# Kernel optimization log

Hardware: AMD Instinct MI355X
Metric: run time of the kernel (lower is better)

Reference implementation:

```python
import jax, jax.numpy as jnp
import numpy as np

N = 80000   # active voxels
G = 64      # voxel grid side
K = 27      # 3x3x3 kernel taps


def _build_coord_maps():
    """Random unique voxel coords in a G^3 grid; 27-tap neighbor index map (-1 = missing)."""
    rng = np.random.default_rng(0)
    flat = rng.choice(G ** 3, size=N, replace=False).astype(np.int64)
    coords = np.stack(np.unravel_index(flat, (G, G, G)), axis=1)  # (N,3)
    order = np.argsort(flat)
    skeys = flat[order]
    offs = [(dx, dy, dz) for dx in (-1, 0, 1) for dy in (-1, 0, 1) for dz in (-1, 0, 1)]
    nbr = np.full((K, N), -1, np.int32)
    for k, (dx, dy, dz) in enumerate(offs):
        nc = coords + np.array([dx, dy, dz])
        inb = np.all((nc >= 0) & (nc < G), axis=1)
        nkey = nc[:, 0] * G * G + nc[:, 1] * G + nc[:, 2]
        pos = np.clip(np.searchsorted(skeys, nkey), 0, N - 1)
        hit = inb & (skeys[pos] == nkey)
        nbr[k] = np.where(hit, order[pos], -1)
    return nbr


_W_SPECS = [('a1w', (27, 96, 64)), ('a2w', (64, 64)), ('a3w', (27, 64, 64)), ('a4w', (64, 64)),
            ('b1w', (27, 256, 64)), ('b2w', (64, 64)), ('b3w', (27, 64, 32)), ('b4w', (32, 32)),
            ('c1w', (27, 96, 128)), ('c2w', (128, 128)), ('c3w', (128, 128))]
_BN_SPECS = [('a1', 64), ('a2', 64), ('a3', 64), ('a4', 64),
             ('b1', 64), ('b2', 64), ('b3', 32), ('b4', 32),
             ('c1', 128), ('c2', 128), ('c3', 128)]


def setup_inputs() -> dict:
    key = jax.random.key(0)
    ks = jax.random.split(key, 64)
    inp = {
        'feat3d': jax.random.normal(ks[0], (N, 96), jnp.float32),
        'feat2d': jax.random.normal(ks[1], (N, 256), jnp.float32),
    }
    i = 2
    for name, shp in _W_SPECS:
        fan = float(np.prod(shp[:-1]))
        inp[name] = jax.random.normal(ks[i], shp, jnp.float32) * (1.0 / np.sqrt(fan))
        i += 1
    for pre, c in _BN_SPECS:  # folded eval-mode BN: y = x*scale + shift
        inp[pre + 's'] = 1.0 + 0.1 * jax.random.normal(ks[i], (c,), jnp.float32)
        inp[pre + 'b'] = 0.1 * jax.random.normal(ks[i + 1], (c,), jnp.float32)
        i += 2
    inp['nbr_idx'] = jnp.asarray(_build_coord_maps())
    inp['align_idx'] = jnp.arange(N, dtype=jnp.int32)  # 2D/3D share coordinates -> exact match
    return inp


def _sconv(x, W, nbr):
    """Sparse 3x3x3 conv: per-tap masked gather + GEMM, accumulated (gather-GEMM-scatter)."""
    out = jnp.zeros((x.shape[0], W.shape[-1]), x.dtype)
    for k in range(W.shape[0]):
        idx = nbr[k]
        g = jnp.where((idx >= 0)[:, None], x[jnp.maximum(idx, 0)], 0.0)
        out = out + g @ W[k]
    return out


def _bnrelu(x, s, b):
    return jax.nn.relu(x * s + b)


def reference(feat3d, feat2d,
              a1w, a2w, a3w, a4w, b1w, b2w, b3w, b4w, c1w, c2w, c3w,
              a1s, a1b, a2s, a2b, a3s, a3b, a4s, a4b,
              b1s, b1b, b2s, b2b, b3s, b3b, b4s, b4b,
              c1s, c1b, c2s, c2b, c3s, c3b,
              nbr_idx, align_idx):
    # 3D branch: 96 -> 64 (dropout = identity in eval)
    x = _bnrelu(_sconv(feat3d, a1w, nbr_idx), a1s, a1b)
    x = _bnrelu(x @ a2w, a2s, a2b)
    x = _bnrelu(_sconv(x, a3w, nbr_idx), a3s, a3b)
    x3 = _bnrelu(x @ a4w, a4s, a4b)
    # 2D branch: 256 -> 32
    y = _bnrelu(_sconv(feat2d, b1w, nbr_idx), b1s, b1b)
    y = _bnrelu(y @ b2w, b2s, b2b)
    y = _bnrelu(_sconv(y, b3w, nbr_idx), b3s, b3b)
    y2 = _bnrelu(y @ b4w, b4s, b4b)
    # features_at_coordinates: exact-match gather at the 3D coords, NaN/Inf -> 0
    ya = y2[align_idx]
    ya = jnp.where(jnp.isfinite(ya), ya, 0.0)
    # fusion: concat 64+32=96 -> 128
    z = jnp.concatenate([x3, ya], axis=1)
    z = _bnrelu(_sconv(z, c1w, nbr_idx), c1s, c1b)
    z = _bnrelu(z @ c2w, c2s, c2b)
    z = _bnrelu(z @ c3w, c3s, c3b)
    return z
```

## Files before the change

kernel.cpp:

```cpp
#include <hip/hip_runtime.h>

typedef __bf16 bf16;
typedef __bf16 bf16x8 __attribute__((ext_vector_type(8)));
typedef __bf16 bf16x4 __attribute__((ext_vector_type(4)));
typedef float  f32x4  __attribute__((ext_vector_type(4)));

__global__ void f2b_kernel(const float* __restrict__ src, bf16* __restrict__ dst, int n4) {
    int i = blockIdx.x * 256 + threadIdx.x;
    if (i >= n4) return;
    float4 v = ((const float4*)src)[i];
    bf16x4 o = { (bf16)v.x, (bf16)v.y, (bf16)v.z, (bf16)v.w };
    ((bf16x4*)dst)[i] = o;
}

__global__ void swz_kernel(const float* __restrict__ W, bf16* __restrict__ Wf,
                           int cin, int cout, int total) {
    int e = blockIdx.x * 256 + threadIdx.x;
    if (e >= total) return;
    int per_tap = cin * cout;
    int tap = e / per_tap;
    int t2  = e - tap * per_tap;
    int ntc = cout >> 4;
    int s   = t2 / (ntc * 512);
    int r3  = t2 - s * (ntc * 512);
    int nt  = r3 >> 9;
    int L   = (r3 & 511) >> 3;
    int j   = r3 & 7;
    int k   = s * 32 + (L >> 4) * 8 + j;
    int col = nt * 16 + (L & 15);
    Wf[e] = (bf16)W[((size_t)tap * cin + k) * cout + col];
}

template<int CIN, int C1, int TAPS, int KTILE, int C2, int C3>
__global__ __launch_bounds__(256, 3) void layer_kernel(
    const bf16* __restrict__ X,
    const bf16* __restrict__ W1,
    const bf16* __restrict__ W2,
    const bf16* __restrict__ W3,
    const int*  __restrict__ nbr,
    const float* __restrict__ sc1, const float* __restrict__ sh1,
    const float* __restrict__ sc2, const float* __restrict__ sh2,
    const float* __restrict__ sc3, const float* __restrict__ sh3,
    bf16* __restrict__ Y, float* __restrict__ Yf,
    int ystride, int yoff, int n, int nblocks)
{
    constexpr int M    = 128;
    constexpr int NT1  = C1 / 16;
    constexpr int WR1  = 4;
    constexpr int WC1  = (NT1 >= 2) ? NT1 / 2 : 1;
    constexpr int KH   = CIN / KTILE;
    constexpr int KS   = KTILE / 32;
    constexpr int CH   = KTILE / 8;
    constexpr int SREG = KTILE / 16;
    constexpr int AST  = KTILE + 8;
    constexpr int ABUF = M * AST;
    constexpr int ABY  = 2 * ABUF * 2;
    constexpr int LS1  = C1 + 8;
    constexpr int LS2  = C2 + 8;
    constexpr int L1BY = M * LS1 * 2;
    constexpr int L2BY = (C3 > 0) ? M * LS2 * 2 : 0;
    constexpr int SBY  = (ABY > L1BY ? (ABY > L2BY ? ABY : L2BY)
                                     : (L1BY > L2BY ? L1BY : L2BY));

    __shared__ __align__(16) char smem[SBY];
    __shared__ int idxs[TAPS * M];
    bf16* As = (bf16*)smem;

    const int tid = threadIdx.x;

    const int bq  = nblocks >> 3, br = nblocks & 7;
    const int bx  = blockIdx.x & 7, bs = blockIdx.x >> 3;
    const int sb  = bx * bq + (bx < br ? bx : br) + bs;
    const int base = sb * M;

    const int lane  = tid & 63;
    const int wv    = tid >> 6;
    const int m16   = lane & 15;
    const int quad  = lane >> 4;
    const int wrow1 = wv & 1;
    const int wcol1 = wv >> 1;

    for (int e = tid; e < TAPS * M; e += 256)
        idxs[e] = nbr[(e >> 7) * n + base + (e & (M - 1))];
    __syncthreads();

    int rr[SREG], cof[SREG], lofs[SREG];
#pragma unroll
    for (int j = 0; j < SREG; ++j) {
        int e = tid + 256 * j;
        rr[j]   = e / CH;
        int c   = e - rr[j] * CH;
        cof[j]  = c * 8;
        lofs[j] = rr[j] * AST + c * 8;
    }

    float4 sreg[SREG];
    auto issue_loads = [&](int kh, int t) {
#pragma unroll
        for (int j = 0; j < SREG; ++j) {
            int idx = idxs[t * M + rr[j]];
            float4 val = {0.f, 0.f, 0.f, 0.f};
            if (idx >= 0) val = *(const float4*)(X + (size_t)idx * CIN + kh * KTILE + cof[j]);
            sreg[j] = val;
        }
    };
    auto store_lds = [&](int buf) {
#pragma unroll
        for (int j = 0; j < SREG; ++j)
            *(float4*)(&As[buf * ABUF + lofs[j]]) = sreg[j];
    };

    f32x4 acc1[WR1][WC1];
#pragma unroll
    for (int r = 0; r < WR1; ++r)
#pragma unroll
        for (int c = 0; c < WC1; ++c) acc1[r][c] = (f32x4){0.f, 0.f, 0.f, 0.f};

    issue_loads(0, 0);
    store_lds(0);

    int it = 0;
    for (int kh = 0; kh < KH; ++kh)
        for (int t = 0; t < TAPS; ++t, ++it) {
            __syncthreads();

            const bf16* wt = W1 + (size_t)t * (CIN * C1);
            bf16x8 bfr[KS][WC1];
#pragma unroll
            for (int s = 0; s < KS; ++s)
#pragma unroll
                for (int c = 0; c < WC1; ++c)
                    bfr[s][c] = *(const bf16x8*)(wt + ((kh * KS + s) * NT1 + wcol1 * WC1 + c) * 512 + lane * 8);

            int t2 = t + 1, kh2 = kh;
            if (t2 == TAPS) { t2 = 0; kh2 = kh + 1; }
            const bool more = (kh2 < KH);
            if (more) issue_loads(kh2, t2);

            const int buf = it & 1;
#pragma unroll
            for (int s = 0; s < KS; ++s) {
                bf16x8 a[WR1];
#pragma unroll
                for (int r = 0; r < WR1; ++r)
                    a[r] = *(const bf16x8*)(&As[buf * ABUF + ((wrow1 * WR1 + r) * 16 + m16) * AST + s * 32 + quad * 8]);
#pragma unroll
                for (int r = 0; r < WR1; ++r)
#pragma unroll
                    for (int c = 0; c < WC1; ++c)
                        acc1[r][c] = __builtin_amdgcn_mfma_f32_16x16x32_bf16(a[r], bfr[s][c], acc1[r][c], 0, 0, 0);
            }

            if (more) store_lds(buf ^ 1);
        }

    __syncthreads();
    bf16* Lt1 = (bf16*)smem;
#pragma unroll
    for (int c = 0; c < WC1; ++c) {
        int col = (wcol1 * WC1 + c) * 16 + m16;
        float s1 = sc1[col], h1 = sh1[col];
#pragma unroll
        for (int r = 0; r < WR1; ++r) {
            int row0 = (wrow1 * WR1 + r) * 16 + quad * 4;
#pragma unroll
            for (int i = 0; i < 4; ++i) {
                float v = acc1[r][c][i] * s1 + h1;
                v = v > 0.f ? v : 0.f;
                Lt1[(row0 + i) * LS1 + col] = (bf16)v;
            }
        }
    }
    __syncthreads();

    constexpr int NT2 = C2 / 16;
    constexpr int WR2 = 4;
    constexpr int WC2 = (NT2 >= 2) ? NT2 / 2 : 1;
    constexpr int KS2 = C1 / 32;
    const int wrow2 = wv & 1, wcol2 = wv >> 1;

    f32x4 acc2[WR2][WC2];
#pragma unroll
    for (int r = 0; r < WR2; ++r)
#pragma unroll
        for (int c = 0; c < WC2; ++c) acc2[r][c] = (f32x4){0.f, 0.f, 0.f, 0.f};

#pragma unroll
    for (int s = 0; s < KS2; ++s) {
        bf16x8 a[WR2], bw[WC2];
#pragma unroll
        for (int r = 0; r < WR2; ++r)
            a[r] = *(const bf16x8*)(&Lt1[((wrow2 * WR2 + r) * 16 + m16) * LS1 + s * 32 + quad * 8]);
#pragma unroll
        for (int c = 0; c < WC2; ++c)
            bw[c] = *(const bf16x8*)(W2 + ((s * NT2 + wcol2 * WC2 + c) * 512 + lane * 8));
#pragma unroll
        for (int r = 0; r < WR2; ++r)
#pragma unroll
            for (int c = 0; c < WC2; ++c)
                acc2[r][c] = __builtin_amdgcn_mfma_f32_16x16x32_bf16(a[r], bw[c], acc2[r][c], 0, 0, 0);
    }

    if constexpr (C3 == 0) {
#pragma unroll
        for (int c = 0; c < WC2; ++c) {
            int col = (wcol2 * WC2 + c) * 16 + m16;
            float s2 = sc2[col], h2 = sh2[col];
#pragma unroll
            for (int r = 0; r < WR2; ++r) {
                int row0 = base + (wrow2 * WR2 + r) * 16 + quad * 4;
#pragma unroll
                for (int i = 0; i < 4; ++i) {
                    float v = acc2[r][c][i] * s2 + h2;
                    v = v > 0.f ? v : 0.f;
                    size_t off = (size_t)(row0 + i) * ystride + yoff + col;
                    if (Yf) Yf[off] = v;
                    else    Y[off] = (bf16)v;
                }
            }
        }
    } else {
        __syncthreads();
        bf16* Lt2 = (bf16*)smem;
#pragma unroll
        for (int c = 0; c < WC2; ++c) {
            int col = (wcol2 * WC2 + c) * 16 + m16;
            float s2 = sc2[col], h2 = sh2[col];
#pragma unroll
            for (int r = 0; r < WR2; ++r) {
                int row0 = (wrow2 * WR2 + r) * 16 + quad * 4;
#pragma unroll
                for (int i = 0; i < 4; ++i) {
                    float v = acc2[r][c][i] * s2 + h2;
                    v = v > 0.f ? v : 0.f;
                    Lt2[(row0 + i) * LS2 + col] = (bf16)v;
                }
            }
        }
        __syncthreads();

        constexpr int C3v = (C3 > 0) ? C3 : 16;
        constexpr int NT3 = C3v / 16;
        constexpr int WR3 = 4;
        constexpr int WC3 = (NT3 >= 2) ? NT3 / 2 : 1;
        constexpr int KS3 = C2 / 32;
        const int wrow3 = wv & 1, wcol3 = wv >> 1;

        f32x4 acc3[WR3][WC3];
#pragma unroll
        for (int r = 0; r < WR3; ++r)
#pragma unroll
            for (int c = 0; c < WC3; ++c) acc3[r][c] = (f32x4){0.f, 0.f, 0.f, 0.f};

#pragma unroll
        for (int s = 0; s < KS3; ++s) {
            bf16x8 a[WR3], bw[WC3];
#pragma unroll
            for (int r = 0; r < WR3; ++r)
                a[r] = *(const bf16x8*)(&Lt2[((wrow3 * WR3 + r) * 16 + m16) * LS2 + s * 32 + quad * 8]);
#pragma unroll
            for (int c = 0; c < WC3; ++c)
                bw[c] = *(const bf16x8*)(W3 + ((s * NT3 + wcol3 * WC3 + c) * 512 + lane * 8));
#pragma unroll
            for (int r = 0; r < WR3; ++r)
#pragma unroll
                for (int c = 0; c < WC3; ++c)
                    acc3[r][c] = __builtin_amdgcn_mfma_f32_16x16x32_bf16(a[r], bw[c], acc3[r][c], 0, 0, 0);
        }

#pragma unroll
        for (int c = 0; c < WC3; ++c) {
            int col = (wcol3 * WC3 + c) * 16 + m16;
            float s3 = sc3[col], h3 = sh3[col];
#pragma unroll
            for (int r = 0; r < WR3; ++r) {
                int row0 = base + (wrow3 * WR3 + r) * 16 + quad * 4;
#pragma unroll
                for (int i = 0; i < 4; ++i) {
                    float v = acc3[r][c][i] * s3 + h3;
                    v = v > 0.f ? v : 0.f;
                    size_t off = (size_t)(row0 + i) * ystride + yoff + col;
                    if (Yf) Yf[off] = v;
                    else    Y[off] = (bf16)v;
                }
            }
        }
    }
}

__global__ void concat_kernel(const bf16* __restrict__ y2, const int* __restrict__ align,
                              bf16* __restrict__ z, int n) {
    int e = blockIdx.x * 256 + threadIdx.x;
    if (e >= n * 32) return;
    int i = e >> 5, c = e & 31;
    int a = align[i];
    float v = (float)y2[(size_t)a * 32 + c];
    unsigned u = __builtin_bit_cast(unsigned, v);
    if ((u & 0x7f800000u) == 0x7f800000u) v = 0.f;
    z[(size_t)i * 96 + 64 + c] = (bf16)v;
}

extern "C" void kernel_launch(void* const* d_in, const int* in_sizes, int n_in,
                              void* d_out, int out_size, void* d_ws, size_t ws_size,
                              hipStream_t stream) {
    const float* feat3d = (const float*)d_in[0];
    const float* feat2d = (const float*)d_in[1];
    const float* Wsrc[11];
    for (int i = 0; i < 11; ++i) Wsrc[i] = (const float*)d_in[2 + i];
    const float* bn[22];
    for (int i = 0; i < 22; ++i) bn[i] = (const float*)d_in[13 + i];
    const int* nbr   = (const int*)d_in[35];
    const int* align = (const int*)d_in[36];
    float* out = (float*)d_out;

    const int n = in_sizes[0] / 96;

    char* ws = (char*)d_ws;
    size_t off = 0;
    auto alloc = [&](size_t bytes) -> void* {
        void* p = ws + off;
        off = (off + bytes + 255) & ~(size_t)255;
        return p;
    };
    bf16* F3 = (bf16*)alloc((size_t)n * 96 * 2);
    bf16* F2 = (bf16*)alloc((size_t)n * 256 * 2);
    static const int wt_taps[11] = {27, 1, 27, 1, 27, 1, 27, 1, 27, 1, 1};
    static const int wt_cin[11]  = {96, 64, 64, 64, 256, 64, 64, 32, 96, 128, 128};
    static const int wt_cout[11] = {64, 64, 64, 64, 64, 64, 32, 32, 128, 128, 128};
    bf16* Wf[11];
    for (int i = 0; i < 11; ++i)
        Wf[i] = (bf16*)alloc((size_t)wt_taps[i] * wt_cin[i] * wt_cout[i] * 2);
    bf16* tA = (bf16*)alloc((size_t)n * 64 * 2);
    bf16* tB = (bf16*)alloc((size_t)n * 64 * 2);
    bf16* y2 = (bf16*)alloc((size_t)n * 32 * 2);
    bf16* z  = (bf16*)alloc((size_t)n * 96 * 2);

    f2b_kernel<<<(n * 96 / 4 + 255) / 256, 256, 0, stream>>>(feat3d, F3, n * 96 / 4);
    f2b_kernel<<<(n * 256 / 4 + 255) / 256, 256, 0, stream>>>(feat2d, F2, n * 256 / 4);
    for (int i = 0; i < 11; ++i) {
        int total = wt_taps[i] * wt_cin[i] * wt_cout[i];
        swz_kernel<<<(total + 255) / 256, 256, 0, stream>>>(Wsrc[i], Wf[i], wt_cin[i], wt_cout[i], total);
    }

    const int GB = n / 128;

    layer_kernel<96, 64, 27, 32, 64, 0><<<GB, 256, 0, stream>>>(
        F3, Wf[0], Wf[1], nullptr, nbr,
        bn[0], bn[1], bn[2], bn[3], nullptr, nullptr,
        tB, nullptr, 64, 0, n, GB);
    layer_kernel<64, 64, 27, 64, 64, 0><<<GB, 256, 0, stream>>>(
        tB, Wf[2], Wf[3], nullptr, nbr,
        bn[4], bn[5], bn[6], bn[7], nullptr, nullptr,
        z, nullptr, 96, 0, n, GB);

    layer_kernel<256, 64, 27, 64, 64, 0><<<GB, 256, 0, stream>>>(
        F2, Wf[4], Wf[5], nullptr, nbr,
        bn[8], bn[9], bn[10], bn[11], nullptr, nullptr,
        tA, nullptr, 64, 0, n, GB);
    layer_kernel<64, 32, 27, 64, 32, 0><<<GB, 256, 0, stream>>>(
        tA, Wf[6], Wf[7], nullptr, nbr,
        bn[12], bn[13], bn[14], bn[15], nullptr, nullptr,
        y2, nullptr, 32, 0, n, GB);

    concat_kernel<<<(n * 32 + 255) / 256, 256, 0, stream>>>(y2, align, z, n);

    layer_kernel<96, 128, 27, 32, 128, 128><<<GB, 256, 0, stream>>>(
        z, Wf[8], Wf[9], Wf[10], nbr,
        bn[16], bn[17], bn[18], bn[19], bn[20], bn[21],
        nullptr, out, 128, 0, n, GB);
}
```

Baseline: 592.1 us.

## Deepen sparse-conv main loop pipeline with double register buffers and weight prefetch

Restructures the tap/K loop of the fused sparse-conv kernel into a two-step unrolled software pipeline. Gathered neighbor rows are fetched two iterations ahead into alternating register sets. Weight fragments are prefetched one iteration ahead instead of being loaded just before the MFMAs. The LDS store now happens before the MMA step rather than after, so global-load latency is hidden behind more compute. The cost is roughly doubled staging and weight registers, which may reduce occupancy or cause spills.

```diff
diff --git a/kernel.cpp b/kernel.cpp
--- a/kernel.cpp
+++ b/kernel.cpp
@@ -61,6 +61,7 @@
     constexpr int L2BY = (C3 > 0) ? M * LS2 * 2 : 0;
     constexpr int SBY  = (ABY > L1BY ? (ABY > L2BY ? ABY : L2BY)
                                      : (L1BY > L2BY ? L1BY : L2BY));
+    constexpr int NIT  = KH * TAPS;
 
     __shared__ __align__(16) char smem[SBY];
     __shared__ int idxs[TAPS * M];
@@ -94,20 +95,27 @@
         lofs[j] = rr[j] * AST + c * 8;
     }
 
-    float4 sreg[SREG];
-    auto issue_loads = [&](int kh, int t) {
+    auto issue_loads = [&](int kh, int t, float4 (&sr)[SREG]) {
 #pragma unroll
         for (int j = 0; j < SREG; ++j) {
             int idx = idxs[t * M + rr[j]];
             float4 val = {0.f, 0.f, 0.f, 0.f};
             if (idx >= 0) val = *(const float4*)(X + (size_t)idx * CIN + kh * KTILE + cof[j]);
-            sreg[j] = val;
-        }
-    };
-    auto store_lds = [&](int buf) {
+            sr[j] = val;
+        }
+    };
+    auto store_lds = [&](int buf, float4 (&sr)[SREG]) {
 #pragma unroll
         for (int j = 0; j < SREG; ++j)
-            *(float4*)(&As[buf * ABUF + lofs[j]]) = sreg[j];
+            *(float4*)(&As[buf * ABUF + lofs[j]]) = sr[j];
+    };
+    auto load_w = [&](int kh, int t, bf16x8 (&bw)[KS][WC1]) {
+        const bf16* wt = W1 + (size_t)t * (CIN * C1);
+#pragma unroll
+        for (int s = 0; s < KS; ++s)
+#pragma unroll
+            for (int c = 0; c < WC1; ++c)
+                bw[s][c] = *(const bf16x8*)(wt + ((kh * KS + s) * NT1 + wcol1 * WC1 + c) * 512 + lane * 8);
     };
 
     f32x4 acc1[WR1][WC1];
@@ -116,43 +124,60 @@
 #pragma unroll
         for (int c = 0; c < WC1; ++c) acc1[r][c] = (f32x4){0.f, 0.f, 0.f, 0.f};
 
-    issue_loads(0, 0);
-    store_lds(0);
-
-    int it = 0;
-    for (int kh = 0; kh < KH; ++kh)
-        for (int t = 0; t < TAPS; ++t, ++it) {
+    auto mma_step = [&](int buf, bf16x8 (&bw)[KS][WC1]) {
+#pragma unroll
+        for (int s = 0; s < KS; ++s) {
+            bf16x8 a[WR1];
+#pragma unroll
+            for (int r = 0; r < WR1; ++r)
+                a[r] = *(const bf16x8*)(&As[buf * ABUF + ((wrow1 * WR1 + r) * 16 + m16) * AST + s * 32 + quad * 8]);
+#pragma unroll
+            for (int r = 0; r < WR1; ++r)
+#pragma unroll
+                for (int c = 0; c < WC1; ++c)
+                    acc1[r][c] = __builtin_amdgcn_mfma_f32_16x16x32_bf16(a[r], bw[s][c], acc1[r][c], 0, 0, 0);
+        }
+    };
+
+    float4 sregA[SREG], sregB[SREG];
+    bf16x8 bfrA[KS][WC1], bfrB[KS][WC1];
+
+    issue_loads(0, 0, sregA);
+    load_w(0, 0, bfrA);
+    store_lds(0, sregA);
+    if (NIT > 1) issue_loads(0, 1, sregB);
+
+    int ts = 2, khs = 0;
+    int tw = 1, khw = 0;
+
+    for (int it = 0; it < NIT; it += 2) {
+        {
             __syncthreads();
-
-            const bf16* wt = W1 + (size_t)t * (CIN * C1);
-            bf16x8 bfr[KS][WC1];
-#pragma unroll
-            for (int s = 0; s < KS; ++s)
-#pragma unroll
-                for (int c = 0; c < WC1; ++c)
-                    bfr[s][c] = *(const bf16x8*)(wt + ((kh * KS + s) * NT1 + wcol1 * WC1 + c) * 512 + lane * 8);
-
-            int t2 = t + 1, kh2 = kh;
-            if (t2 == TAPS) { t2 = 0; kh2 = kh + 1; }
-            const bool more = (kh2 < KH);
-            if (more) issue_loads(kh2, t2);
-
-            const int buf = it & 1;
-#pragma unroll
-            for (int s = 0; s < KS; ++s) {
-                bf16x8 a[WR1];
-#pragma unroll
-                for (int r = 0; r < WR1; ++r)
-                    a[r] = *(const bf16x8*)(&As[buf * ABUF + ((wrow1 * WR1 + r) * 16 + m16) * AST + s * 32 + quad * 8]);
-#pragma unroll
-                for (int r = 0; r < WR1; ++r)
-#pragma unroll
-                    for (int c = 0; c < WC1; ++c)
-                        acc1[r][c] = __builtin_amdgcn_mfma_f32_16x16x32_bf16(a[r], bfr[s][c], acc1[r][c], 0, 0, 0);
-            }
-
-            if (more) store_lds(buf ^ 1);
-        }
+            if (it + 1 < NIT) store_lds(1, sregB);
+            if (it + 2 < NIT) {
+                issue_loads(khs, ts, sregA);
+                if (++ts == TAPS) { ts = 0; ++khs; }
+            }
+            if (it + 1 < NIT) {
+                load_w(khw, tw, bfrB);
+                if (++tw == TAPS) { tw = 0; ++khw; }
+            }
+            mma_step(0, bfrA);
+        }
+        if (it + 1 < NIT) {
+            __syncthreads();
+            if (it + 2 < NIT) store_lds(0, sregA);
+            if (it + 3 < NIT) {
+                issue_loads(khs, ts, sregB);
+                if (++ts == TAPS) { ts = 0; ++khs; }
+            }
+            if (it + 2 < NIT) {
+                load_w(khw, tw, bfrA);
+                if (++tw == TAPS) { tw = 0; ++khw; }
+            }
+            mma_step(1, bfrB);
+        }
+    }
 
     __syncthreads();
     bf16* Lt1 = (bf16*)smem;
```

Result: slower. 620.6 us (+4.8%).

## Use single-wave blocks with register-direct gathered A operands and double-buffered prefetch

Applied to the files above, without the earlier changes.

Replaces the 4-wave, 128-row, LDS-staged gather kernel with a one-wavefront block that owns 64 rows (32 for the 128-channel layer). Each lane loads its neighbor rows straight into MFMA A registers, and A operands, weight fragments and neighbor indices are prefetched one step ahead in ping-pong register buffers. All __syncthreads and LDS staging for the conv phase go away, and LDS is now used only for the pointwise epilogue layers. The cost is more weight-fragment loads per row (no sharing across waves), higher register pressure, and reliance on many small blocks for occupancy.

```diff
diff --git a/kernel.cpp b/kernel.cpp
--- a/kernel.cpp
+++ b/kernel.cpp
@@ -31,8 +31,8 @@
     Wf[e] = (bf16)W[((size_t)tap * cin + k) * cout + col];
 }
 
-template<int CIN, int C1, int TAPS, int KTILE, int C2, int C3>
-__global__ __launch_bounds__(256, 3) void layer_kernel(
+template<int CIN, int C1, int TAPS, int C2, int C3>
+__global__ __launch_bounds__(64, 2) void layer_kernel(
     const bf16* __restrict__ X,
     const bf16* __restrict__ W1,
     const bf16* __restrict__ W2,
@@ -44,70 +44,40 @@
     bf16* __restrict__ Y, float* __restrict__ Yf,
     int ystride, int yoff, int n, int nblocks)
 {
-    constexpr int M    = 128;
-    constexpr int NT1  = C1 / 16;
-    constexpr int WR1  = 4;
-    constexpr int WC1  = (NT1 >= 2) ? NT1 / 2 : 1;
-    constexpr int KH   = CIN / KTILE;
-    constexpr int KS   = KTILE / 32;
-    constexpr int CH   = KTILE / 8;
-    constexpr int SREG = KTILE / 16;
-    constexpr int AST  = KTILE + 8;
-    constexpr int ABUF = M * AST;
-    constexpr int ABY  = 2 * ABUF * 2;
-    constexpr int LS1  = C1 + 8;
-    constexpr int LS2  = C2 + 8;
-    constexpr int L1BY = M * LS1 * 2;
-    constexpr int L2BY = (C3 > 0) ? M * LS2 * 2 : 0;
-    constexpr int SBY  = (ABY > L1BY ? (ABY > L2BY ? ABY : L2BY)
-                                     : (L1BY > L2BY ? L1BY : L2BY));
-
-    __shared__ __align__(16) char smem[SBY];
-    __shared__ int idxs[TAPS * M];
-    bf16* As = (bf16*)smem;
-
-    const int tid = threadIdx.x;
-
-    const int bq  = nblocks >> 3, br = nblocks & 7;
-    const int bx  = blockIdx.x & 7, bs = blockIdx.x >> 3;
-    const int sb  = bx * bq + (bx < br ? bx : br) + bs;
-    const int base = sb * M;
-
-    const int lane  = tid & 63;
-    const int wv    = tid >> 6;
-    const int m16   = lane & 15;
-    const int quad  = lane >> 4;
-    const int wrow1 = wv & 1;
-    const int wcol1 = wv >> 1;
-
-    for (int e = tid; e < TAPS * M; e += 256)
-        idxs[e] = nbr[(e >> 7) * n + base + (e & (M - 1))];
-    __syncthreads();
-
-    int rr[SREG], cof[SREG], lofs[SREG];
-#pragma unroll
-    for (int j = 0; j < SREG; ++j) {
-        int e = tid + 256 * j;
-        rr[j]   = e / CH;
-        int c   = e - rr[j] * CH;
-        cof[j]  = c * 8;
-        lofs[j] = rr[j] * AST + c * 8;
-    }
-
-    float4 sreg[SREG];
-    auto issue_loads = [&](int kh, int t) {
-#pragma unroll
-        for (int j = 0; j < SREG; ++j) {
-            int idx = idxs[t * M + rr[j]];
-            float4 val = {0.f, 0.f, 0.f, 0.f};
-            if (idx >= 0) val = *(const float4*)(X + (size_t)idx * CIN + kh * KTILE + cof[j]);
-            sreg[j] = val;
-        }
+    constexpr int NT1 = C1 / 16;
+    constexpr int WC1 = NT1;
+    constexpr int WR1 = (C1 >= 128) ? 2 : 4;
+    constexpr int RW  = WR1 * 16;
+    constexpr int KS  = CIN / 32;
+    constexpr int TOT = TAPS * KS;
+    constexpr int LS1 = C1 + 8;
+    constexpr int LS2 = C2 + 8;
+    constexpr int LSM = (LS1 > LS2) ? LS1 : LS2;
+
+    __shared__ __align__(16) bf16 Lt[RW * LSM];
+
+    const int lane = threadIdx.x;
+    const int m16  = lane & 15;
+    const int quad = lane >> 4;
+
+    const int bq = nblocks >> 3, br = nblocks & 7;
+    const int bx = blockIdx.x & 7, bs = blockIdx.x >> 3;
+    const int sb = bx * bq + (bx < br ? bx : br) + bs;
+    const int base = sb * RW;
+
+    const bf16x8 ZB = __builtin_bit_cast(bf16x8, (float4){0.f, 0.f, 0.f, 0.f});
+
+    int idxc[WR1], idxn[WR1];
+    auto load_idx = [&](int t, int (&id)[WR1]) {
+#pragma unroll
+        for (int r = 0; r < WR1; ++r)
+            id[r] = nbr[(size_t)t * n + base + r * 16 + m16];
     };
-    auto store_lds = [&](int buf) {
-#pragma unroll
-        for (int j = 0; j < SREG; ++j)
-            *(float4*)(&As[buf * ABUF + lofs[j]]) = sreg[j];
+    auto load_b = [&](int step, bf16x8 (&b)[WC1]) {
+        const bf16* wt = W1 + (size_t)step * (NT1 * 512) + lane * 8;
+#pragma unroll
+        for (int c = 0; c < WC1; ++c)
+            b[c] = *(const bf16x8*)(wt + c * 512);
     };
 
     f32x4 acc1[WR1][WC1];
@@ -116,86 +86,90 @@
 #pragma unroll
         for (int c = 0; c < WC1; ++c) acc1[r][c] = (f32x4){0.f, 0.f, 0.f, 0.f};
 
-    issue_loads(0, 0);
-    store_lds(0);
-
-    int it = 0;
-    for (int kh = 0; kh < KH; ++kh)
-        for (int t = 0; t < TAPS; ++t, ++it) {
-            __syncthreads();
-
-            const bf16* wt = W1 + (size_t)t * (CIN * C1);
-            bf16x8 bfr[KS][WC1];
-#pragma unroll
-            for (int s = 0; s < KS; ++s)
-#pragma unroll
-                for (int c = 0; c < WC1; ++c)
-                    bfr[s][c] = *(const bf16x8*)(wt + ((kh * KS + s) * NT1 + wcol1 * WC1 + c) * 512 + lane * 8);
-
-            int t2 = t + 1, kh2 = kh;
-            if (t2 == TAPS) { t2 = 0; kh2 = kh + 1; }
-            const bool more = (kh2 < KH);
-            if (more) issue_loads(kh2, t2);
-
-            const int buf = it & 1;
-#pragma unroll
-            for (int s = 0; s < KS; ++s) {
-                bf16x8 a[WR1];
-#pragma unroll
-                for (int r = 0; r < WR1; ++r)
-                    a[r] = *(const bf16x8*)(&As[buf * ABUF + ((wrow1 * WR1 + r) * 16 + m16) * AST + s * 32 + quad * 8]);
-#pragma unroll
-                for (int r = 0; r < WR1; ++r)
-#pragma unroll
-                    for (int c = 0; c < WC1; ++c)
-                        acc1[r][c] = __builtin_amdgcn_mfma_f32_16x16x32_bf16(a[r], bfr[s][c], acc1[r][c], 0, 0, 0);
-            }
-
-            if (more) store_lds(buf ^ 1);
-        }
-
-    __syncthreads();
-    bf16* Lt1 = (bf16*)smem;
+    bf16x8 aA[WR1], aB[WR1], bA[WC1], bB[WC1];
+
+    load_idx(0, idxc);
+    load_idx(1, idxn);
+    load_b(0, bA);
+#pragma unroll
+    for (int r = 0; r < WR1; ++r) {
+        bf16x8 v = ZB;
+        int id_ = idxc[r];
+        if (id_ >= 0) v = *(const bf16x8*)(X + (unsigned)id_ * CIN + quad * 8);
+        aA[r] = v;
+    }
+
+    int t = 0, s = 0;
+    auto step = [&](int it, bf16x8 (&aC)[WR1], bf16x8 (&bC)[WC1],
+                    bf16x8 (&aN)[WR1], bf16x8 (&bN)[WC1]) {
+        int s1 = s + 1, t1 = t;
+        bool wrap = (s1 == KS);
+        if (wrap) { s1 = 0; ++t1; }
+        if (it + 1 < TOT) {
+            load_b(t1 * KS + s1, bN);
+#pragma unroll
+            for (int r = 0; r < WR1; ++r) {
+                int id_ = wrap ? idxn[r] : idxc[r];
+                bf16x8 v = ZB;
+                if (id_ >= 0) v = *(const bf16x8*)(X + (unsigned)id_ * CIN + s1 * 32 + quad * 8);
+                aN[r] = v;
+            }
+        }
+#pragma unroll
+        for (int r = 0; r < WR1; ++r)
+#pragma unroll
+            for (int c = 0; c < WC1; ++c)
+                acc1[r][c] = __builtin_amdgcn_mfma_f32_16x16x32_bf16(aC[r], bC[c], acc1[r][c], 0, 0, 0);
+        if (wrap) {
+#pragma unroll
+            for (int r = 0; r < WR1; ++r) idxc[r] = idxn[r];
+            if (t + 2 < TAPS) load_idx(t + 2, idxn);
+        }
+        t = t1; s = s1;
+    };
+
+    for (int it = 0; it < TOT; it += 2) {
+        step(it, aA, bA, aB, bB);
+        if (it + 1 < TOT) step(it + 1, aB, bB, aA, bA);
+    }
+
 #pragma unroll
     for (int c = 0; c < WC1; ++c) {
-        int col = (wcol1 * WC1 + c) * 16 + m16;
-        float s1 = sc1[col], h1 = sh1[col];
+        int col = c * 16 + m16;
+        float sc = sc1[col], sh = sh1[col];
 #pragma unroll
         for (int r = 0; r < WR1; ++r) {
-            int row0 = (wrow1 * WR1 + r) * 16 + quad * 4;
+            int row0 = r * 16 + quad * 4;
 #pragma unroll
             for (int i = 0; i < 4; ++i) {
-                float v = acc1[r][c][i] * s1 + h1;
+                float v = acc1[r][c][i] * sc + sh;
                 v = v > 0.f ? v : 0.f;
-                Lt1[(row0 + i) * LS1 + col] = (bf16)v;
-            }
-        }
-    }
-    __syncthreads();
+                Lt[(row0 + i) * LS1 + col] = (bf16)v;
+            }
+        }
+    }
 
     constexpr int NT2 = C2 / 16;
-    constexpr int WR2 = 4;
-    constexpr int WC2 = (NT2 >= 2) ? NT2 / 2 : 1;
+    constexpr int WC2 = NT2;
     constexpr int KS2 = C1 / 32;
-    const int wrow2 = wv & 1, wcol2 = wv >> 1;
-
-    f32x4 acc2[WR2][WC2];
-#pragma unroll
-    for (int r = 0; r < WR2; ++r)
+
+    f32x4 acc2[WR1][WC2];
+#pragma unroll
+    for (int r = 0; r < WR1; ++r)
 #pragma unroll
         for (int c = 0; c < WC2; ++c) acc2[r][c] = (f32x4){0.f, 0.f, 0.f, 0.f};
 
 #pragma unroll
-    for (int s = 0; s < KS2; ++s) {
-        bf16x8 a[WR2], bw[WC2];
-#pragma unroll
-        for (int r = 0; r < WR2; ++r)
-            a[r] = *(const bf16x8*)(&Lt1[((wrow2 * WR2 + r) * 16 + m16) * LS1 + s * 32 + quad * 8]);
+    for (int s2 = 0; s2 < KS2; ++s2) {
+        bf16x8 a[WR1], bw[WC2];
+#pragma unroll
+        for (int r = 0; r < WR1; ++r)
+            a[r] = *(const bf16x8*)(&Lt[(r * 16 + m16) * LS1 + s2 * 32 + quad * 8]);
 #pragma unroll
         for (int c = 0; c < WC2; ++c)
-            bw[c] = *(const bf16x8*)(W2 + ((s * NT2 + wcol2 * WC2 + c) * 512 + lane * 8));
-#pragma unroll
-        for (int r = 0; r < WR2; ++r)
+            bw[c] = *(const bf16x8*)(W2 + ((s2 * NT2 + c) * 512 + lane * 8));
+#pragma unroll
+        for (int r = 0; r < WR1; ++r)
 #pragma unroll
             for (int c = 0; c < WC2; ++c)
                 acc2[r][c] = __builtin_amdgcn_mfma_f32_16x16x32_bf16(a[r], bw[c], acc2[r][c], 0, 0, 0);
@@ -204,14 +178,14 @@
     if constexpr (C3 == 0) {
 #pragma unroll
         for (int c = 0; c < WC2; ++c) {
-            int col = (wcol2 * WC2 + c) * 16 + m16;
-            float s2 = sc2[col], h2 = sh2[col];
-#pragma unroll
-            for (int r = 0; r < WR2; ++r) {
-                int row0 = base + (wrow2 * WR2 + r) * 16 + quad * 4;
+            int col = c * 16 + m16;
+            float sc = sc2[col], sh = sh2[col];
+#pragma unroll
+            for (int r = 0; r < WR1; ++r) {
+                int row0 = base + r * 16 + quad * 4;
 #pragma unroll
                 for (int i = 0; i < 4; ++i) {
-                    float v = acc2[r][c][i] * s2 + h2;
+                    float v = acc2[r][c][i] * sc + sh;
                     v = v > 0.f ? v : 0.f;
                     size_t off = (size_t)(row0 + i) * ystride + yoff + col;
                     if (Yf) Yf[off] = v;
@@ -220,49 +194,44 @@
             }
         }
     } else {
-        __syncthreads();
-        bf16* Lt2 = (bf16*)smem;
 #pragma unroll
         for (int c = 0; c < WC2; ++c) {
-            int col = (wcol2 * WC2 + c) * 16 + m16;
-            float s2 = sc2[col], h2 = sh2[col];
-#pragma unroll
-            for (int r = 0; r < WR2; ++r) {
-                int row0 = (wrow2 * WR2 + r) * 16 + quad * 4;
+            int col = c * 16 + m16;
+            float sc = sc2[col], sh = sh2[col];
+#pragma unroll
+            for (int r = 0; r < WR1; ++r) {
+                int row0 = r * 16 + quad * 4;
 #pragma unroll
                 for (int i = 0; i < 4; ++i) {
-                    float v = acc2[r][c][i] * s2 + h2;
+                    float v = acc2[r][c][i] * sc + sh;
                     v = v > 0.f ? v : 0.f;
-                    Lt2[(row0 + i) * LS2 + col] = (bf16)v;
+                    Lt[(row0 + i) * LS2 + col] = (bf16)v;
                 }
             }
         }
-        __syncthreads();
 
         constexpr int C3v = (C3 > 0) ? C3 : 16;
         constexpr int NT3 = C3v / 16;
-        constexpr int WR3 = 4;
-        constexpr int WC3 = (NT3 >= 2) ? NT3 / 2 : 1;
+        constexpr int WC3 = NT3;
         constexpr int KS3 = C2 / 32;
-        const int wrow3 = wv & 1, wcol3 = wv >> 1;
-
-        f32x4 acc3[WR3][WC3];
-#pragma unroll
-        for (int r = 0; r < WR3; ++r)
+
+        f32x4 acc3[WR1][WC3];
+#pragma unroll
+        for (int r = 0; r < WR1; ++r)
 #pragma unroll
             for (int c = 0; c < WC3; ++c) acc3[r][c] = (f32x4){0.f, 0.f, 0.f, 0.f};
 
 #pragma unroll
-        for (int s = 0; s < KS3; ++s) {
-            bf16x8 a[WR3], bw[WC3];
-#pragma unroll
-            for (int r = 0; r < WR3; ++r)
-                a[r] = *(const bf16x8*)(&Lt2[((wrow3 * WR3 + r) * 16 + m16) * LS2 + s * 32 + quad * 8]);
+        for (int s3 = 0; s3 < KS3; ++s3) {
+            bf16x8 a[WR1], bw[WC3];
+#pragma unroll
+            for (int r = 0; r < WR1; ++r)
+                a[r] = *(const bf16x8*)(&Lt[(r * 16 + m16) * LS2 + s3 * 32 + quad * 8]);
 #pragma unroll
             for (int c = 0; c < WC3; ++c)
-                bw[c] = *(const bf16x8*)(W3 + ((s * NT3 + wcol3 * WC3 + c) * 512 + lane * 8));
-#pragma unroll
-            for (int r = 0; r < WR3; ++r)
+                bw[c] = *(const bf16x8*)(W3 + ((s3 * NT3 + c) * 512 + lane * 8));
+#pragma unroll
+            for (int r = 0; r < WR1; ++r)
 #pragma unroll
                 for (int c = 0; c < WC3; ++c)
                     acc3[r][c] = __builtin_amdgcn_mfma_f32_16x16x32_bf16(a[r], bw[c], acc3[r][c], 0, 0, 0);
@@ -270,14 +239,14 @@
 
 #pragma unroll
         for (int c = 0; c < WC3; ++c) {
-            int col = (wcol3 * WC3 + c) * 16 + m16;
-            float s3 = sc3[col], h3 = sh3[col];
-#pragma unroll
-            for (int r = 0; r < WR3; ++r) {
-                int row0 = base + (wrow3 * WR3 + r) * 16 + quad * 4;
+            int col = c * 16 + m16;
+            float sc = sc3[col], sh = sh3[col];
+#pragma unroll
+            for (int r = 0; r < WR1; ++r) {
+                int row0 = base + r * 16 + quad * 4;
 #pragma unroll
                 for (int i = 0; i < 4; ++i) {
-                    float v = acc3[r][c][i] * s3 + h3;
+                    float v = acc3[r][c][i] * sc + sh;
                     v = v > 0.f ? v : 0.f;
                     size_t off = (size_t)(row0 + i) * ystride + yoff + col;
                     if (Yf) Yf[off] = v;
@@ -342,30 +311,31 @@
         swz_kernel<<<(total + 255) / 256, 256, 0, stream>>>(Wsrc[i], Wf[i], wt_cin[i], wt_cout[i], total);
     }
 
-    const int GB = n / 128;
-
-    layer_kernel<96, 64, 27, 32, 64, 0><<<GB, 256, 0, stream>>>(
+    const int GB64 = n / 64;
+    const int GB32 = n / 32;
+
+    layer_kernel<96, 64, 27, 64, 0><<<GB64, 64, 0, stream>>>(
         F3, Wf[0], Wf[1], nullptr, nbr,
         bn[0], bn[1], bn[2], bn[3], nullptr, nullptr,
-        tB, nullptr, 64, 0, n, GB);
-    layer_kernel<64, 64, 27, 64, 64, 0><<<GB, 256, 0, stream>>>(
+        tB, nullptr, 64, 0, n, GB64);
+    layer_kernel<64, 64, 27, 64, 0><<<GB64, 64, 0, stream>>>(
         tB, Wf[2], Wf[3], nullptr, nbr,
         bn[4], bn[5], bn[6], bn[7], nullptr, nullptr,
-        z, nullptr, 96, 0, n, GB);
-
-    layer_kernel<256, 64, 27, 64, 64, 0><<<GB, 256, 0, stream>>>(
+        z, nullptr, 96, 0, n, GB64);
+
+    layer_kernel<256, 64, 27, 64, 0><<<GB64, 64, 0, stream>>>(
         F2, Wf[4], Wf[5], nullptr, nbr,
         bn[8], bn[9], bn[10], bn[11], nullptr, nullptr,
-        tA, nullptr, 64, 0, n, GB);
-    layer_kernel<64, 32, 27, 64, 32, 0><<<GB, 256, 0, stream>>>(
+        tA, nullptr, 64, 0, n, GB64);
+    layer_kernel<64, 32, 27, 32, 0><<<GB64, 64, 0, stream>>>(
         tA, Wf[6], Wf[7], nullptr, nbr,
         bn[12], bn[13], bn[14], bn[15], nullptr, nullptr,
-        y2, nullptr, 32, 0, n, GB);
+        y2, nullptr, 32, 0, n, GB64);
 
     concat_kernel<<<(n * 32 + 255) / 256, 256, 0, stream>>>(y2, align, z, n);
 
-    layer_kernel<96, 128, 27, 32, 128, 128><<<GB, 256, 0, stream>>>(
+    layer_kernel<96, 128, 27, 128, 128><<<GB32, 64, 0, stream>>>(
         z, Wf[8], Wf[9], Wf[10], nbr,
         bn[16], bn[17], bn[18], bn[19], bn[20], bn[21],
-        nullptr, out, 128, 0, n, GB);
-}
+        nullptr, out, 128, 0, n, GB32);
+}
```

After: 631.1 us. 1.07x slower.
